# Kernel tuning notes

Measured on AMD Instinct MI355X. Metric: run time of the kernel, lower is better.

The kernel has to match this reference:

```python
import jax, jax.numpy as jnp
import numpy as np

B, N, FIN, F = 512, 512, 2, 128  # batch, n_sites, input features, hidden features


def setup_inputs() -> dict:
    key = jax.random.key(0)
    k1, k2 = jax.random.split(key)
    inputs = jax.random.normal(k1, (B, N, FIN), dtype=jnp.float32)
    # LSTM dense kernel over concat([inputs_i, hidden]) -> 4*F gates (i, f, g, o)
    Wk = jax.random.normal(k2, (FIN + F, 4 * F), dtype=jnp.float32) / np.sqrt(FIN + F)
    b = jnp.zeros((4 * F,), dtype=jnp.float32)
    return {"inputs": inputs, "Wk": Wk, "b": b}


def reference(inputs, Wk, b):
    # exclusive=True, reorder_idx=None: inputs_i = 0 at k=0, else inputs[:, k-1, :];
    # memory state = outputs[:, k-1, :] = previous hidden (zeros buffer at k=0).
    batch = inputs.shape[0]
    x_shift = jnp.concatenate(
        [jnp.zeros_like(inputs[:, :1, :]), inputs[:, :-1, :]], axis=1
    )  # (B, N, FIN)
    xs = jnp.swapaxes(x_shift, 0, 1)  # (N, B, FIN) scan over sites

    c0 = jnp.zeros((batch, F), dtype=inputs.dtype)
    h0 = jnp.zeros((batch, F), dtype=inputs.dtype)

    def step(carry, x_t):
        c, h = carry
        ifgo = jnp.concatenate([x_t, h], axis=-1) @ Wk + b  # (B, 4F)
        i, f, g, o = jnp.split(ifgo, 4, axis=-1)
        c = jax.nn.sigmoid(f) * c + jax.nn.sigmoid(i) * jnp.tanh(g)
        h = jax.nn.sigmoid(o) * jnp.tanh(c)
        return (c, h), h

    _, hs = jax.lax.scan(step, (c0, h0), xs)  # hs: (N, B, F)
    outputs = jnp.swapaxes(hs, 0, 1)  # (B, N, F)
    return outputs
```

## Files before the change

kernel.cpp:

```cpp
#include <hip/hip_runtime.h>

#define B_   512
#define N_   512
#define FIN_ 2
#define F_   128
#define G_   512
#define XSTRIDE 1040
#define H8STRIDE 320

typedef int         int4_   __attribute__((ext_vector_type(4)));
typedef float       float4_ __attribute__((ext_vector_type(4)));
typedef float       float2_ __attribute__((ext_vector_type(2)));

#define LOG2E_  1.44269504f
#define LOG2E2_ 2.88539008f

__global__ void __launch_bounds__(256)
lstm_prep(const float* __restrict__ Wk, const float* __restrict__ bias,
          signed char* __restrict__ qw, float* __restrict__ sc)
{
    const int col = blockIdx.x * 256 + threadIdx.x;
    float cm = 1e-20f;
    for (int k = 0; k < F_; ++k)
        cm = fmaxf(cm, fabsf(Wk[(size_t)(2 + k) * G_ + col]));
    const float scale = 127.f / cm;
    sc[col * 4 + 0] = Wk[col];
    sc[col * 4 + 1] = Wk[G_ + col];
    sc[col * 4 + 2] = bias[col];
    sc[col * 4 + 3] = cm / (127.f * 127.f);
    for (int k = 0; k < F_; ++k) {
        const float wv = Wk[(size_t)(2 + k) * G_ + col] * scale;
        int q = (int)rintf(wv);
        q = q > 127 ? 127 : (q < -127 ? -127 : q);
        qw[col * F_ + k] = (signed char)q;
    }
}

template<bool PF>
__device__ __forceinline__ void lstm_step(
    const signed char* hsrc,
    signed char* hdst,
    float* outp,
    const int4_ (&wq)[4][2], const float (&invs)[4],
    const float (&w0r)[4], const float (&w1r)[4], const float (&br)[4],
    int4_ (&acc)[4], float2_ xv, float& cs, int grp,
    const float* xpf, float2_& pf1, float2_& pf2)
{
    const int4_ a0 = *reinterpret_cast<const int4_*>(hsrc + grp * 16);
    const int4_ a1 = *reinterpret_cast<const int4_*>(hsrc + 64 + grp * 16);

    if (PF) {
        pf1 = *reinterpret_cast<const float2_*>(xpf);
        pf2 = *reinterpret_cast<const float2_*>(xpf + 2);
    }

    float xp[4];
#pragma unroll
    for (int t = 0; t < 4; ++t)
        xp[t] = fmaf(xv[0], w0r[t], fmaf(xv[1], w1r[t], br[t]));

#pragma unroll
    for (int t = 0; t < 4; ++t) acc[t][0] = 0;

    acc[2] = __builtin_amdgcn_mfma_i32_16x16x64_i8(a0, wq[2][0], acc[2], 0, 0, 0);
    acc[0] = __builtin_amdgcn_mfma_i32_16x16x64_i8(a0, wq[0][0], acc[0], 0, 0, 0);
    acc[1] = __builtin_amdgcn_mfma_i32_16x16x64_i8(a0, wq[1][0], acc[1], 0, 0, 0);
    acc[3] = __builtin_amdgcn_mfma_i32_16x16x64_i8(a0, wq[3][0], acc[3], 0, 0, 0);
    acc[2] = __builtin_amdgcn_mfma_i32_16x16x64_i8(a1, wq[2][1], acc[2], 0, 0, 0);
    acc[0] = __builtin_amdgcn_mfma_i32_16x16x64_i8(a1, wq[0][1], acc[0], 0, 0, 0);
    acc[1] = __builtin_amdgcn_mfma_i32_16x16x64_i8(a1, wq[1][1], acc[1], 0, 0, 0);
    acc[3] = __builtin_amdgcn_mfma_i32_16x16x64_i8(a1, wq[3][1], acc[3], 0, 0, 0);

    const float pg = fmaf((float)acc[2][0], invs[2], xp[2]);
    const float pi = fmaf((float)acc[0][0], invs[0], xp[0]);
    const float pf_ = fmaf((float)acc[1][0], invs[1], xp[1]);
    const float eg = __builtin_amdgcn_exp2f(LOG2E2_ * pg);
    const float ei = __builtin_amdgcn_exp2f(-LOG2E_ * pi);
    const float ef = __builtin_amdgcn_exp2f(-LOG2E_ * pf_);
    const float rg = __builtin_amdgcn_rcpf(1.f + eg);
    const float ri = __builtin_amdgcn_rcpf(1.f + ei);
    const float rf = __builtin_amdgcn_rcpf(1.f + ef);
    const float gg = fmaf(-2.f, rg, 1.f);
    cs = fmaf(rf, cs, ri * gg);
    const float po = fmaf((float)acc[3][0], invs[3], xp[3]);
    const float eo = __builtin_amdgcn_exp2f(-LOG2E_ * po);
    const float ec = __builtin_amdgcn_exp2f(LOG2E2_ * cs);
    const float ro = __builtin_amdgcn_rcpf(1.f + eo);
    const float rc = __builtin_amdgcn_rcpf(1.f + ec);
    const float h = fmaf(-2.f * ro, rc, ro);

    const int q = (int)rintf(h * 127.f);
    *hdst = (signed char)q;
    *outp = h;
    asm volatile("s_waitcnt lgkmcnt(0)\n\ts_barrier" ::: "memory");
}

__global__ void __launch_bounds__(512)
lstm_scan(const float* __restrict__ inp, const signed char* __restrict__ qw,
          const float* __restrict__ sc, float* __restrict__ out)
{
    const int bb   = blockIdx.x;
    const int tid  = threadIdx.x;
    const int w    = tid >> 6;
    const int lane = tid & 63;
    const int c15  = lane & 15;
    const int grp  = lane >> 4;

    __shared__ __align__(16) signed char h8[2][4 * H8STRIDE];
    __shared__ __align__(64) float x_lds[2 * XSTRIDE];

    float w0r[4], w1r[4], br[4], invs[4];
    int4_ wq[4][2];
#pragma unroll
    for (int t = 0; t < 4; ++t) {
        const int col = t * F_ + w * 16 + c15;
        const float4_ s = *reinterpret_cast<const float4_*>(sc + col * 4);
        w0r[t] = s[0]; w1r[t] = s[1]; br[t] = s[2]; invs[t] = s[3];
#pragma unroll
        for (int i = 0; i < 2; ++i)
            wq[t][i] = *reinterpret_cast<const int4_*>(qw + col * F_ + i * 64 + grp * 16);
    }

    {
        const float* xsrc = inp + (size_t)(2 * bb) * (N_ * FIN_);
        const int i4 = tid * 4;
        float4_ v = *reinterpret_cast<const float4_*>(xsrc + i4);
        const int row = i4 >> 10, idx = i4 & 1023;
        *reinterpret_cast<float4_*>(&x_lds[row * XSTRIDE + idx]) = v;
    }
    for (int i = tid; i < 2 * 4 * H8STRIDE; i += 512)
        ((signed char*)h8)[i] = 0;
    __syncthreads();

    const int r    = (lane >> 4) & 1;
    const int hrow = (c15 >> 2) & 1;
    const int wrow = r + ((lane >> 5) << 1);

    const signed char* hr0 = &h8[0][hrow * H8STRIDE];
    const signed char* hr1 = &h8[1][hrow * H8STRIDE];
    signed char* hw0 = &h8[0][wrow * H8STRIDE + w * 16 + c15];
    signed char* hw1 = &h8[1][wrow * H8STRIDE + w * 16 + c15];
    const float* xq = &x_lds[r * XSTRIDE];
    float* outp = out + (size_t)(2 * bb + r) * N_ * F_ + w * 16 + c15;

    float cs = 0.f;
    int4_ acc[4];
#pragma unroll
    for (int t = 0; t < 4; ++t) { acc[t][0] = 0; acc[t][1] = 0; acc[t][2] = 0; acc[t][3] = 0; }

    float2_ xz; xz[0] = 0.f; xz[1] = 0.f;
    float2_ pf1, pf2;

    lstm_step<true>(hr0, hw1, outp, wq, invs, w0r, w1r, br, acc, xz, cs, grp,
                    xq, pf1, pf2);
    outp += F_;

    for (int i = 0; i < 255; ++i) {
        const float2_ xv1 = pf1;
        const float2_ xv2 = pf2;
        lstm_step<true>(hr1, hw0, outp, wq, invs, w0r, w1r, br, acc, xv1, cs,
                        grp, xq + 4 * i + 4, pf1, pf2);
        outp += F_;
        lstm_step<false>(hr0, hw1, outp, wq, invs, w0r, w1r, br, acc, xv2, cs,
                         grp, nullptr, pf1, pf2);
        outp += F_;
    }
    lstm_step<false>(hr1, hw0, outp, wq, invs, w0r, w1r, br, acc, pf1, cs,
                     grp, nullptr, pf1, pf2);
}

extern "C" void kernel_launch(void* const* d_in, const int* in_sizes, int n_in,
                              void* d_out, int out_size, void* d_ws, size_t ws_size,
                              hipStream_t stream) {
    const float* inp  = (const float*)d_in[0];
    const float* Wk   = (const float*)d_in[1];
    const float* bias = (const float*)d_in[2];
    float* out        = (float*)d_out;
    signed char* qw = (signed char*)d_ws;
    float* sc       = (float*)((char*)d_ws + 64 * 1024);
    lstm_prep<<<dim3(2), dim3(256), 0, stream>>>(Wk, bias, qw, sc);
    lstm_scan<<<dim3(B_ / 2), dim3(512), 0, stream>>>(inp, qw, sc, out);
}
```

Before: 228.4 us.

## Split LSTM gate activations across wave halves and exchange via ds_bpermute

Lanes 0-31 and 32-63 previously computed identical rows, each evaluating all four gate activations. Now the lower half evaluates the input and forget gates while the upper half evaluates the cell and output gates, and the results are swapped with ds_bpermute. This halves the exp and rcp work per lane on the serial per-step path. The log2e and sign factors are folded into the precomputed scale table, and only the lower half writes outputs. The cost is an added cross-lane LDS permute round trip inside each recurrent step, which sits on the critical latency chain.

```diff
diff --git a/kernel.cpp b/kernel.cpp
--- a/kernel.cpp
+++ b/kernel.cpp
@@ -20,14 +20,16 @@
           signed char* __restrict__ qw, float* __restrict__ sc)
 {
     const int col = blockIdx.x * 256 + threadIdx.x;
+    const int g = col >> 7;
+    const float sgn = (g == 2) ? LOG2E2_ : -LOG2E_;
     float cm = 1e-20f;
     for (int k = 0; k < F_; ++k)
         cm = fmaxf(cm, fabsf(Wk[(size_t)(2 + k) * G_ + col]));
     const float scale = 127.f / cm;
-    sc[col * 4 + 0] = Wk[col];
-    sc[col * 4 + 1] = Wk[G_ + col];
-    sc[col * 4 + 2] = bias[col];
-    sc[col * 4 + 3] = cm / (127.f * 127.f);
+    sc[col * 4 + 0] = sgn * Wk[col];
+    sc[col * 4 + 1] = sgn * Wk[G_ + col];
+    sc[col * 4 + 2] = sgn * bias[col];
+    sc[col * 4 + 3] = sgn * (cm / (127.f * 127.f));
     for (int k = 0; k < F_; ++k) {
         const float wv = Wk[(size_t)(2 + k) * G_ + col] * scale;
         int q = (int)rintf(wv);
@@ -41,9 +43,8 @@
     const signed char* hsrc,
     signed char* hdst,
     float* outp,
-    const int4_ (&wq)[4][2], const float (&invs)[4],
-    const float (&w0r)[4], const float (&w1r)[4], const float (&br)[4],
-    int4_ (&acc)[4], float2_ xv, float& cs, int grp,
+    const int4_ (&wq)[4][2], const int4_& z4, const float (&scl)[8],
+    float2_ xv, float& cs, int grp, int bpaddr, bool lo32,
     const float* xpf, float2_& pf1, float2_& pf2)
 {
     const int4_ a0 = *reinterpret_cast<const int4_*>(hsrc + grp * 16);
@@ -54,44 +55,39 @@
         pf2 = *reinterpret_cast<const float2_*>(xpf + 2);
     }
 
-    float xp[4];
-#pragma unroll
-    for (int t = 0; t < 4; ++t)
-        xp[t] = fmaf(xv[0], w0r[t], fmaf(xv[1], w1r[t], br[t]));
+    const float xpA = fmaf(xv[0], scl[0], fmaf(xv[1], scl[1], scl[2]));
+    const float xpB = fmaf(xv[0], scl[4], fmaf(xv[1], scl[5], scl[6]));
 
-#pragma unroll
-    for (int t = 0; t < 4; ++t) acc[t][0] = 0;
+    int4_ acc0 = __builtin_amdgcn_mfma_i32_16x16x64_i8(a0, wq[0][0], z4, 0, 0, 0);
+    int4_ acc2 = __builtin_amdgcn_mfma_i32_16x16x64_i8(a0, wq[2][0], z4, 0, 0, 0);
+    int4_ acc1 = __builtin_amdgcn_mfma_i32_16x16x64_i8(a0, wq[1][0], z4, 0, 0, 0);
+    int4_ acc3 = __builtin_amdgcn_mfma_i32_16x16x64_i8(a0, wq[3][0], z4, 0, 0, 0);
+    acc0 = __builtin_amdgcn_mfma_i32_16x16x64_i8(a1, wq[0][1], acc0, 0, 0, 0);
+    acc2 = __builtin_amdgcn_mfma_i32_16x16x64_i8(a1, wq[2][1], acc2, 0, 0, 0);
+    acc1 = __builtin_amdgcn_mfma_i32_16x16x64_i8(a1, wq[1][1], acc1, 0, 0, 0);
+    acc3 = __builtin_amdgcn_mfma_i32_16x16x64_i8(a1, wq[3][1], acc3, 0, 0, 0);
 
-    acc[2] = __builtin_amdgcn_mfma_i32_16x16x64_i8(a0, wq[2][0], acc[2], 0, 0, 0);
-    acc[0] = __builtin_amdgcn_mfma_i32_16x16x64_i8(a0, wq[0][0], acc[0], 0, 0, 0);
-    acc[1] = __builtin_amdgcn_mfma_i32_16x16x64_i8(a0, wq[1][0], acc[1], 0, 0, 0);
-    acc[3] = __builtin_amdgcn_mfma_i32_16x16x64_i8(a0, wq[3][0], acc[3], 0, 0, 0);
-    acc[2] = __builtin_amdgcn_mfma_i32_16x16x64_i8(a1, wq[2][1], acc[2], 0, 0, 0);
-    acc[0] = __builtin_amdgcn_mfma_i32_16x16x64_i8(a1, wq[0][1], acc[0], 0, 0, 0);
-    acc[1] = __builtin_amdgcn_mfma_i32_16x16x64_i8(a1, wq[1][1], acc[1], 0, 0, 0);
-    acc[3] = __builtin_amdgcn_mfma_i32_16x16x64_i8(a1, wq[3][1], acc[3], 0, 0, 0);
-
-    const float pg = fmaf((float)acc[2][0], invs[2], xp[2]);
-    const float pi = fmaf((float)acc[0][0], invs[0], xp[0]);
-    const float pf_ = fmaf((float)acc[1][0], invs[1], xp[1]);
-    const float eg = __builtin_amdgcn_exp2f(LOG2E2_ * pg);
-    const float ei = __builtin_amdgcn_exp2f(-LOG2E_ * pi);
-    const float ef = __builtin_amdgcn_exp2f(-LOG2E_ * pf_);
-    const float rg = __builtin_amdgcn_rcpf(1.f + eg);
-    const float ri = __builtin_amdgcn_rcpf(1.f + ei);
-    const float rf = __builtin_amdgcn_rcpf(1.f + ef);
-    const float gg = fmaf(-2.f, rg, 1.f);
-    cs = fmaf(rf, cs, ri * gg);
-    const float po = fmaf((float)acc[3][0], invs[3], xp[3]);
-    const float eo = __builtin_amdgcn_exp2f(-LOG2E_ * po);
+    const int sA = lo32 ? acc0[0] : acc2[0];
+    const int sB = lo32 ? acc1[0] : acc3[0];
+    const float pA = fmaf((float)sA, scl[3], xpA);
+    const float pB = fmaf((float)sB, scl[7], xpB);
+    const float eA = __builtin_amdgcn_exp2f(pA);
+    const float eB = __builtin_amdgcn_exp2f(pB);
+    const float rA = __builtin_amdgcn_rcpf(1.f + eA);
+    const float rB = __builtin_amdgcn_rcpf(1.f + eB);
+    const float g1 = fmaf(-2.f, rA, 1.f);
+    const int qg = __builtin_amdgcn_ds_bpermute(bpaddr, __float_as_int(g1));
+    const int qo = __builtin_amdgcn_ds_bpermute(bpaddr, __float_as_int(rB));
+    const float gg = __int_as_float(qg);
+    const float ro = __int_as_float(qo);
+    cs = fmaf(rB, cs, rA * gg);
     const float ec = __builtin_amdgcn_exp2f(LOG2E2_ * cs);
-    const float ro = __builtin_amdgcn_rcpf(1.f + eo);
     const float rc = __builtin_amdgcn_rcpf(1.f + ec);
     const float h = fmaf(-2.f * ro, rc, ro);
 
     const int q = (int)rintf(h * 127.f);
     *hdst = (signed char)q;
-    *outp = h;
+    if (lo32) *outp = h;
     asm volatile("s_waitcnt lgkmcnt(0)\n\ts_barrier" ::: "memory");
 }
 
@@ -105,20 +101,28 @@
     const int lane = tid & 63;
     const int c15  = lane & 15;
     const int grp  = lane >> 4;
+    const bool lo32 = lane < 32;
+    const int bpaddr = (lane ^ 32) << 2;
 
     __shared__ __align__(16) signed char h8[2][4 * H8STRIDE];
     __shared__ __align__(64) float x_lds[2 * XSTRIDE];
 
-    float w0r[4], w1r[4], br[4], invs[4];
     int4_ wq[4][2];
 #pragma unroll
     for (int t = 0; t < 4; ++t) {
         const int col = t * F_ + w * 16 + c15;
-        const float4_ s = *reinterpret_cast<const float4_*>(sc + col * 4);
-        w0r[t] = s[0]; w1r[t] = s[1]; br[t] = s[2]; invs[t] = s[3];
 #pragma unroll
         for (int i = 0; i < 2; ++i)
             wq[t][i] = *reinterpret_cast<const int4_*>(qw + col * F_ + i * 64 + grp * 16);
+    }
+    float scl[8];
+    {
+        const int tA = lo32 ? 0 : 2;
+        const int colA = tA * F_ + w * 16 + c15;
+        const float4_ sa = *reinterpret_cast<const float4_*>(sc + colA * 4);
+        const float4_ sb = *reinterpret_cast<const float4_*>(sc + (colA + F_) * 4);
+        scl[0] = sa[0]; scl[1] = sa[1]; scl[2] = sa[2]; scl[3] = sa[3];
+        scl[4] = sb[0]; scl[5] = sb[1]; scl[6] = sb[2]; scl[7] = sb[3];
     }
 
     {
@@ -144,29 +148,26 @@
     float* outp = out + (size_t)(2 * bb + r) * N_ * F_ + w * 16 + c15;
 
     float cs = 0.f;
-    int4_ acc[4];
-#pragma unroll
-    for (int t = 0; t < 4; ++t) { acc[t][0] = 0; acc[t][1] = 0; acc[t][2] = 0; acc[t][3] = 0; }
-
+    const int4_ z4 = {0, 0, 0, 0};
     float2_ xz; xz[0] = 0.f; xz[1] = 0.f;
     float2_ pf1, pf2;
 
-    lstm_step<true>(hr0, hw1, outp, wq, invs, w0r, w1r, br, acc, xz, cs, grp,
+    lstm_step<true>(hr0, hw1, outp, wq, z4, scl, xz, cs, grp, bpaddr, lo32,
                     xq, pf1, pf2);
     outp += F_;
 
     for (int i = 0; i < 255; ++i) {
         const float2_ xv1 = pf1;
         const float2_ xv2 = pf2;
-        lstm_step<true>(hr1, hw0, outp, wq, invs, w0r, w1r, br, acc, xv1, cs,
-                        grp, xq + 4 * i + 4, pf1, pf2);
+        lstm_step<true>(hr1, hw0, outp, wq, z4, scl, xv1, cs, grp, bpaddr,
+                        lo32, xq + 4 * i + 4, pf1, pf2);
         outp += F_;
-        lstm_step<false>(hr0, hw1, outp, wq, invs, w0r, w1r, br, acc, xv2, cs,
-                         grp, nullptr, pf1, pf2);
+        lstm_step<false>(hr0, hw1, outp, wq, z4, scl, xv2, cs, grp, bpaddr,
+                         lo32, nullptr, pf1, pf2);
         outp += F_;
     }
-    lstm_step<false>(hr1, hw0, outp, wq, invs, w0r, w1r, br, acc, pf1, cs,
-                     grp, nullptr, pf1, pf2);
+    lstm_step<false>(hr1, hw0, outp, wq, z4, scl, pf1, cs, grp, bpaddr,
+                     lo32, nullptr, pf1, pf2);
 }
 
 extern "C" void kernel_launch(void* const* d_in, const int* in_sizes, int n_in,
```

Measured after the change: 206.6 us (median of 2 runs). -9.5%, faster.
